# Performance work log

Hardware: AMD Instinct MI355X
Metric: run time of the kernel (lower is better)

## Reference

```python
import jax, jax.numpy as jnp
import numpy as np

N = 50000      # nodes
E = 1_000_000  # edges (avg degree 20)
D = 64         # hidden dim
L = 3          # num dynamics layers
LN_EPS = 1e-5


def layernorm(h, g, b):
    mu = jnp.mean(h, axis=-1, keepdims=True)
    var = jnp.mean(jnp.square(h - mu), axis=-1, keepdims=True)
    return (h - mu) * jax.lax.rsqrt(var + LN_EPS) * g + b


def transformer_conv(h, src, dst, Wq, bq, Wk, bk, Wv, bv, Ws, bs):
    # PyG TransformerConv, heads=1, concat=False, beta=False, root_weight=True
    n = h.shape[0]
    d = Wq.shape[1]
    q = h @ Wq + bq            # [N, D] queries (dst side)
    k = h @ Wk + bk            # [N, D] keys   (src side)
    v = h @ Wv + bv            # [N, D] values (src side)
    logits = jnp.sum(q[dst] * k[src], axis=-1) / jnp.sqrt(jnp.asarray(d, h.dtype))  # [E]
    # segment softmax over incoming edges of each dst node
    m = jax.ops.segment_max(logits, dst, num_segments=n)      # [N]
    e = jnp.exp(logits - m[dst])                               # [E]
    s = jax.ops.segment_sum(e, dst, num_segments=n)            # [N]
    a = e / s[dst]                                             # [E]
    agg = jax.ops.segment_sum(a[:, None] * v[src], dst, num_segments=n)  # [N, D]
    return agg + h @ Ws + bs   # root/skip connection


def setup_inputs() -> dict:
    key = jax.random.key(0)
    ks = jax.random.split(key, 24)
    w = lambda k, shape: (jax.random.normal(k, shape, jnp.float32) * 0.05)
    inp = {
        "x": jax.random.normal(ks[0], (N, D), jnp.float32),
        "edge_index": jax.random.randint(ks[1], (2, E), 0, N, jnp.int32),
        # input_proj conv params
        "Wq0": w(ks[2], (D, D)), "bq0": w(ks[3], (D,)),
        "Wk0": w(ks[4], (D, D)), "bk0": w(ks[5], (D,)),
        "Wv0": w(ks[6], (D, D)), "bv0": w(ks[7], (D,)),
        "Ws0": w(ks[8], (D, D)), "bs0": w(ks[9], (D,)),
        "ln0_g": jnp.ones((D,), jnp.float32), "ln0_b": jnp.zeros((D,), jnp.float32),
        # stacked dynamics conv params [L, ...]
        "Wq": w(ks[10], (L, D, D)), "bq": w(ks[11], (L, D)),
        "Wk": w(ks[12], (L, D, D)), "bk": w(ks[13], (L, D)),
        "Wv": w(ks[14], (L, D, D)), "bv": w(ks[15], (L, D)),
        "Ws": w(ks[16], (L, D, D)), "bs": w(ks[17], (L, D)),
        "ln_g": jnp.ones((L, D), jnp.float32), "ln_b": jnp.zeros((L, D), jnp.float32),
    }
    return inp


def reference(x, edge_index, Wq0, bq0, Wk0, bk0, Wv0, bv0, Ws0, bs0, ln0_g, ln0_b,
              Wq, bq, Wk, bk, Wv, bv, Ws, bs, ln_g, ln_b):
    src, dst = edge_index[0], edge_index[1]
    h = transformer_conv(x, src, dst, Wq0, bq0, Wk0, bk0, Wv0, bv0, Ws0, bs0)
    h = jax.nn.relu(layernorm(h, ln0_g, ln0_b))
    # dropout is identity in eval mode
    for i in range(L):
        hi = transformer_conv(h, src, dst, Wq[i], bq[i], Wk[i], bk[i],
                              Wv[i], bv[i], Ws[i], bs[i])
        h = jax.nn.relu(layernorm(hi + h, ln_g[i], ln_b[i]))
    return h
```

## Files before the change

### kernel.cpp

```cpp
#include <hip/hip_runtime.h>
#include <math.h>


#define DD 64
#define NB_HIST 256

typedef __attribute__((ext_vector_type(8))) _Float16 h8;
typedef __attribute__((ext_vector_type(2))) _Float16 h2;
typedef __attribute__((ext_vector_type(4))) float f32x4;

__device__ __forceinline__ unsigned short f2h(float f) {
    union { _Float16 h; unsigned short u; } c;
    c.h = (_Float16)f;
    return c.u;
}
__device__ __forceinline__ h2 u2h2(unsigned u) {
    union { unsigned u; h2 h; } c; c.u = u; return c.h;
}
__device__ __forceinline__ unsigned pk2u(float a, float b) {
    union { decltype(__builtin_amdgcn_cvt_pkrtz(0.f, 0.f)) h; unsigned u; } c;
    c.h = __builtin_amdgcn_cvt_pkrtz(a, b);
    return c.u;
}
__device__ __forceinline__ float h2dot(h2 a, h2 b, float c) {
#if __has_builtin(__builtin_amdgcn_fdot2)
    return __builtin_amdgcn_fdot2(a, b, c, false);
#else
    return fmaf((float)a[0], (float)b[0], fmaf((float)a[1], (float)b[1], c));
#endif
}

__global__ __launch_bounds__(1024) void hist_blk(const int* __restrict__ dst,
                                                 unsigned* __restrict__ cb,
                                                 int E, int nbw) {
    extern __shared__ unsigned hist[];
    int blk = blockIdx.x;
    for (int w = threadIdx.x; w < nbw; w += blockDim.x) hist[w] = 0;
    __syncthreads();
    int chunk = (E + gridDim.x - 1) / gridDim.x;
    int beg = blk * chunk;
    int end = min(E, beg + chunk);
    for (int e = beg + (int)threadIdx.x; e < end; e += blockDim.x) {
        int d = dst[e];
        atomicAdd(&hist[d >> 1], (d & 1) ? 0x10000u : 1u);
    }
    __syncthreads();
    unsigned* out = cb + (size_t)blk * nbw;
    for (int w = threadIdx.x; w < nbw; w += blockDim.x) out[w] = hist[w];
}

__global__ __launch_bounds__(256) void prefix_blk(unsigned* __restrict__ cb,
                                                  int* __restrict__ counts,
                                                  int nbw, int n) {
    int w = blockIdx.x * blockDim.x + threadIdx.x;
    if (w >= nbw) return;
    unsigned acc = 0;
#pragma unroll 1
    for (int c = 0; c < NB_HIST; c += 16) {
        unsigned t[16];
#pragma unroll
        for (int j = 0; j < 16; ++j) t[j] = cb[(size_t)(c + j) * nbw + w];
#pragma unroll
        for (int j = 0; j < 16; ++j) {
            unsigned v = t[j];
            cb[(size_t)(c + j) * nbw + w] = acc;
            acc += v;
        }
    }
    counts[2 * w] = (int)(acc & 0xffffu);
    int b1 = 2 * w + 1;
    if (b1 < n) counts[b1] = (int)(acc >> 16);
}

__global__ __launch_bounds__(1024) void scan_local(const int* __restrict__ counts,
                                                   int* __restrict__ localscan,
                                                   int* __restrict__ blockSums, int n) {
    __shared__ int sh[1024];
    int i = blockIdx.x * 1024 + threadIdx.x;
    int val = (i < n) ? counts[i] : 0;
    sh[threadIdx.x] = val;
    __syncthreads();
    for (int off = 1; off < 1024; off <<= 1) {
        int t = (threadIdx.x >= off) ? sh[threadIdx.x - off] : 0;
        __syncthreads();
        sh[threadIdx.x] += t;
        __syncthreads();
    }
    if (i < n) localscan[i] = sh[threadIdx.x] - val;
    if (threadIdx.x == 1023) blockSums[blockIdx.x] = sh[1023];
}

__global__ __launch_bounds__(64) void scan_tops(int* __restrict__ blockSums, int nb) {
    int i = threadIdx.x;
    int val = (i < nb) ? blockSums[i] : 0;
    int s = val;
#pragma unroll
    for (int off = 1; off < 64; off <<= 1) {
        int t = __shfl_up(s, off, 64);
        if (i >= off) s += t;
    }
    if (i < nb) blockSums[i] = s - val;
}

__global__ void emit_rowptr(const int* __restrict__ localscan,
                            const int* __restrict__ blockSums,
                            int* __restrict__ row_ptr, int n, int E) {
    int i = blockIdx.x * blockDim.x + threadIdx.x;
    if (i < n) row_ptr[i] = localscan[i] + blockSums[i >> 10];
    if (i == 0) row_ptr[n] = E;
}

__global__ __launch_bounds__(1024) void scatter2(const int* __restrict__ src,
                                                 const int* __restrict__ dst,
                                                 const unsigned* __restrict__ cb,
                                                 const int* __restrict__ row_ptr,
                                                 int* __restrict__ col, int E, int nbw) {
    extern __shared__ unsigned hist[];
    int blk = blockIdx.x;
    for (int w = threadIdx.x; w < nbw; w += blockDim.x) hist[w] = 0;
    __syncthreads();
    const unsigned* pref = cb + (size_t)blk * nbw;
    int chunk = (E + gridDim.x - 1) / gridDim.x;
    int beg = blk * chunk;
    int end = min(E, beg + chunk);
    for (int e = beg + (int)threadIdx.x; e < end; e += blockDim.x) {
        int d = dst[e];
        unsigned sh = (unsigned)(d & 1) * 16u;
        unsigned old = atomicAdd(&hist[d >> 1], 1u << sh);
        unsigned lr = (old >> sh) & 0xffffu;
        unsigned pre = (pref[d >> 1] >> sh) & 0xffffu;
        int slot = row_ptr[d] + (int)pre + (int)lr;
        __builtin_nontemporal_store(src[e] << 8, &col[slot]);
    }
}

__global__ void prep_all(const float* __restrict__ x, unsigned short* __restrict__ hbf,
                         int nD,
                         const float* __restrict__ W0, const float* __restrict__ W1,
                         const float* __restrict__ W2, const float* __restrict__ W3,
                         const float* __restrict__ Wqs, const float* __restrict__ Wks,
                         const float* __restrict__ Wvs, const float* __restrict__ Wss,
                         unsigned short* __restrict__ Wt) {
    int i = blockIdx.x * blockDim.x + threadIdx.x;
    if (i < nD) { hbf[i] = f2h(x[i]); return; }
    int id = i - nD;
    if (id >= 16 * 4096) return;
    int mat = id >> 12, rem = id & 4095;
    int nn = rem >> 6, kk = rem & 63;
    int layer = mat >> 2, wh = mat & 3;
    const float* W;
    if (layer == 0) W = wh == 0 ? W0 : wh == 1 ? W1 : wh == 2 ? W2 : W3;
    else {
        const float* base = wh == 0 ? Wqs : wh == 1 ? Wks : wh == 2 ? Wvs : Wss;
        W = base + (size_t)(layer - 1) * 4096;
    }
    float val = W[kk * 64 + nn];
    if (wh == 0) val *= 0.125f;
    Wt[id] = f2h(val);
}

__global__ __launch_bounds__(256) void gemm_mfma(
    const unsigned short* __restrict__ hbf, const unsigned short* __restrict__ Wt,
    const float* __restrict__ Bq, const float* __restrict__ Bk,
    const float* __restrict__ Bv, const float* __restrict__ Bs,
    const float* __restrict__ hprev,
    unsigned short* __restrict__ qO, unsigned short* __restrict__ kvO,
    unsigned short* __restrict__ sO, int ntiles) {
    int lane = threadIdx.x & 63;
    int wave = threadIdx.x >> 6;
    int ml = lane & 15, ql = lane >> 4;

    const unsigned short* W = Wt + wave * 4096;
    h8 wfrag[4][2];
#pragma unroll
    for (int t = 0; t < 4; ++t)
#pragma unroll
        for (int kh = 0; kh < 2; ++kh)
            wfrag[t][kh] = *(const h8*)(W + (t * 16 + ml) * 64 + kh * 32 + ql * 8);

    const float* bias = wave == 0 ? Bq : wave == 1 ? Bk : wave == 2 ? Bv : Bs;
    float4 bias4[4];
#pragma unroll
    for (int t = 0; t < 4; ++t) {
        bias4[t] = *(const float4*)(bias + t * 16 + ql * 4);
        if (wave == 0) {
            bias4[t].x *= 0.125f; bias4[t].y *= 0.125f;
            bias4[t].z *= 0.125f; bias4[t].w *= 0.125f;
        }
    }

    for (int tile = blockIdx.x; tile < ntiles; tile += gridDim.x) {
        int node0 = tile * 16;
        h8 hfrag[2];
#pragma unroll
        for (int kh = 0; kh < 2; ++kh)
            hfrag[kh] = *(const h8*)(hbf + (size_t)(node0 + ml) * 64 + kh * 32 + ql * 8);
        f32x4 acc[4];
#pragma unroll
        for (int t = 0; t < 4; ++t) {
            acc[t][0] = bias4[t].x; acc[t][1] = bias4[t].y;
            acc[t][2] = bias4[t].z; acc[t][3] = bias4[t].w;
        }
#pragma unroll
        for (int t = 0; t < 4; ++t)
#pragma unroll
            for (int kh = 0; kh < 2; ++kh)
                acc[t] = __builtin_amdgcn_mfma_f32_16x16x32_f16(
                    wfrag[t][kh], hfrag[kh], acc[t], 0, 0, 0);

        size_t rowe = (size_t)(node0 + ml) * 64;
        if (wave == 0) {
#pragma unroll
            for (int t = 0; t < 4; ++t) {
                uint2 st;
                st.x = pk2u(acc[t][0], acc[t][1]);
                st.y = pk2u(acc[t][2], acc[t][3]);
                *(uint2*)(qO + rowe + t * 16 + ql * 4) = st;
            }
        } else if (wave == 3) {
#pragma unroll
            for (int t = 0; t < 4; ++t) {
                float4 st = {acc[t][0], acc[t][1], acc[t][2], acc[t][3]};
                if (hprev) {
                    float4 h4 = *(const float4*)(hprev + rowe + t * 16 + ql * 4);
                    st.x += h4.x; st.y += h4.y; st.z += h4.z; st.w += h4.w;
                }
                uint2 sp;
                sp.x = pk2u(st.x, st.y);
                sp.y = pk2u(st.z, st.w);
                *(uint2*)(sO + rowe + t * 16 + ql * 4) = sp;
            }
        } else {
            size_t kve = (size_t)(node0 + ml) * 128 + (wave == 2 ? 64 : 0);
#pragma unroll
            for (int t = 0; t < 4; ++t) {
                uint2 st;
                st.x = pk2u(acc[t][0], acc[t][1]);
                st.y = pk2u(acc[t][2], acc[t][3]);
                *(uint2*)(kvO + kve + t * 16 + ql * 4) = st;
            }
        }
    }
}

#define EDGE_COMP(KU, VU) do {                                                 \
    float d = h2dot(u2h2(qu.x), u2h2((KU).x), 0.0f);                           \
    d = h2dot(u2h2(qu.y), u2h2((KU).y), d);                                    \
    d = h2dot(u2h2(qu.z), u2h2((KU).z), d);                                    \
    d = h2dot(u2h2(qu.w), u2h2((KU).w), d);                                    \
    d += __shfl_xor(d, 1); d += __shfl_xor(d, 2); d += __shfl_xor(d, 4);       \
    float p = __expf(d); ssum += p;                                            \
    h2 v0 = u2h2((VU).x), v1 = u2h2((VU).y), v2 = u2h2((VU).z), v3 = u2h2((VU).w); \
    aa.x = fmaf((float)v0[0], p, aa.x); aa.y = fmaf((float)v0[1], p, aa.y);    \
    aa.z = fmaf((float)v1[0], p, aa.z); aa.w = fmaf((float)v1[1], p, aa.w);    \
    ab.x = fmaf((float)v2[0], p, ab.x); ab.y = fmaf((float)v2[1], p, ab.y);    \
    ab.z = fmaf((float)v3[0], p, ab.z); ab.w = fmaf((float)v3[1], p, ab.w);    \
} while (0)

__global__ __launch_bounds__(256) void attn_agg_ln(
    const unsigned short* __restrict__ qh, const unsigned short* __restrict__ kv,
    const unsigned short* __restrict__ sk,
    const int* __restrict__ row_ptr, const int* __restrict__ col,
    const float* __restrict__ g, const float* __restrict__ b,
    float* __restrict__ out, unsigned short* __restrict__ hbf_out, int n) {
    int node = blockIdx.x * 4 + (threadIdx.x >> 6);
    int lane = threadIdx.x & 63;
    if (node >= n) return;
    int grp = lane >> 3;
    int qi = lane & 7;

    size_t ro = (size_t)node * DD + qi * 8;
    uint4 qu = *(const uint4*)(qh + ro);
    uint4 su = *(const uint4*)(sk + ro);
    int beg = row_ptr[node], end = row_ptr[node + 1];

    float ssum = 0.0f;
    float4 aa = {0.f, 0.f, 0.f, 0.f}, ab = {0.f, 0.f, 0.f, 0.f};
    const char* kvb = (const char*)kv;

    int e = beg + grp;
    int cv0 = (e < end) ? col[e] : -1;
    int cv1 = (e + 8 < end) ? col[e + 8] : -1;
    int cv2 = (e + 16 < end) ? col[e + 16] : -1;
    int cv3 = (e + 24 < end) ? col[e + 24] : -1;
    for (int e0 = beg; e0 < end; e0 += 32) {
        bool a0 = cv0 >= 0, a1 = cv1 >= 0, a2 = cv2 >= 0, a3 = cv3 >= 0;
        uint4 ku0, vu0, ku1, vu1, ku2, vu2, ku3, vu3;
        if (a0) { const uint4* kp = (const uint4*)(kvb + cv0) + qi; ku0 = kp[0]; vu0 = kp[8]; }
        if (a1) { const uint4* kp = (const uint4*)(kvb + cv1) + qi; ku1 = kp[0]; vu1 = kp[8]; }
        if (a2) { const uint4* kp = (const uint4*)(kvb + cv2) + qi; ku2 = kp[0]; vu2 = kp[8]; }
        if (a3) { const uint4* kp = (const uint4*)(kvb + cv3) + qi; ku3 = kp[0]; vu3 = kp[8]; }
        e += 32;
        cv0 = (e < end) ? col[e] : -1;
        cv1 = (e + 8 < end) ? col[e + 8] : -1;
        cv2 = (e + 16 < end) ? col[e + 16] : -1;
        cv3 = (e + 24 < end) ? col[e + 24] : -1;
        if (a0) EDGE_COMP(ku0, vu0);
        if (a1) EDGE_COMP(ku1, vu1);
        if (a2) EDGE_COMP(ku2, vu2);
        if (a3) EDGE_COMP(ku3, vu3);
    }

#pragma unroll
    for (int off = 8; off <= 32; off <<= 1) {
        ssum += __shfl_xor(ssum, off);
        aa.x += __shfl_xor(aa.x, off); aa.y += __shfl_xor(aa.y, off);
        aa.z += __shfl_xor(aa.z, off); aa.w += __shfl_xor(aa.w, off);
        ab.x += __shfl_xor(ab.x, off); ab.y += __shfl_xor(ab.y, off);
        ab.z += __shfl_xor(ab.z, off); ab.w += __shfl_xor(ab.w, off);
    }
    float inv = (end > beg) ? 1.0f / ssum : 0.0f;
    aa.x *= inv; aa.y *= inv; aa.z *= inv; aa.w *= inv;
    ab.x *= inv; ab.y *= inv; ab.z *= inv; ab.w *= inv;

    {
        h2 t0 = u2h2(su.x), t1 = u2h2(su.y), t2 = u2h2(su.z), t3 = u2h2(su.w);
        aa.x += (float)t0[0]; aa.y += (float)t0[1];
        aa.z += (float)t1[0]; aa.w += (float)t1[1];
        ab.x += (float)t2[0]; ab.y += (float)t2[1];
        ab.z += (float)t3[0]; ab.w += (float)t3[1];
    }

    float s1 = aa.x + aa.y + aa.z + aa.w + ab.x + ab.y + ab.z + ab.w;
    s1 += __shfl_xor(s1, 1);
    s1 += __shfl_xor(s1, 2);
    s1 += __shfl_xor(s1, 4);
    float mu = s1 * (1.0f / DD);
    float dx0 = aa.x - mu, dx1 = aa.y - mu, dx2 = aa.z - mu, dx3 = aa.w - mu;
    float dx4 = ab.x - mu, dx5 = ab.y - mu, dx6 = ab.z - mu, dx7 = ab.w - mu;
    float s2v = dx0 * dx0 + dx1 * dx1 + dx2 * dx2 + dx3 * dx3
              + dx4 * dx4 + dx5 * dx5 + dx6 * dx6 + dx7 * dx7;
    s2v += __shfl_xor(s2v, 1);
    s2v += __shfl_xor(s2v, 2);
    s2v += __shfl_xor(s2v, 4);
    float var = s2v * (1.0f / DD);
    float is = rsqrtf(var + 1e-5f);
    float4 g4a = *(const float4*)(g + qi * 8);
    float4 g4b = *(const float4*)(g + qi * 8 + 4);
    float4 b4a = *(const float4*)(b + qi * 8);
    float4 b4b = *(const float4*)(b + qi * 8 + 4);
    float4 ya, yb;
    ya.x = fmaxf(dx0 * is * g4a.x + b4a.x, 0.0f);
    ya.y = fmaxf(dx1 * is * g4a.y + b4a.y, 0.0f);
    ya.z = fmaxf(dx2 * is * g4a.z + b4a.z, 0.0f);
    ya.w = fmaxf(dx3 * is * g4a.w + b4a.w, 0.0f);
    yb.x = fmaxf(dx4 * is * g4b.x + b4b.x, 0.0f);
    yb.y = fmaxf(dx5 * is * g4b.y + b4b.y, 0.0f);
    yb.z = fmaxf(dx6 * is * g4b.z + b4b.z, 0.0f);
    yb.w = fmaxf(dx7 * is * g4b.w + b4b.w, 0.0f);
    if (grp == 0) {
        *(float4*)(out + ro) = ya;
        *(float4*)(out + ro + 4) = yb;
        uint4 hv;
        hv.x = pk2u(ya.x, ya.y);
        hv.y = pk2u(ya.z, ya.w);
        hv.z = pk2u(yb.x, yb.y);
        hv.w = pk2u(yb.z, yb.w);
        *(uint4*)(hbf_out + ro) = hv;
    }
}

extern "C" void kernel_launch(void* const* d_in, const int* in_sizes, int n_in,
                              void* d_out, int out_size, void* d_ws, size_t ws_size,
                              hipStream_t stream) {
    const int D = DD;
    const float* x = (const float*)d_in[0];
    const int n = in_sizes[0] / D;
    const int* ei = (const int*)d_in[1];
    const int E = in_sizes[1] / 2;
    const int* srcp = ei;
    const int* dstp = ei + E;
    const int nbw = (n + 1) / 2;

    static bool s_attr = false;
    if (!s_attr) {
        s_attr = true;
        (void)hipFuncSetAttribute((const void*)hist_blk,
                                  hipFuncAttributeMaxDynamicSharedMemorySize, 102400);
        (void)hipFuncSetAttribute((const void*)scatter2,
                                  hipFuncAttributeMaxDynamicSharedMemorySize, 102400);
    }

    char* wsp = (char*)d_ws;
    auto take = [&](size_t bytes) {
        char* p = wsp;
        wsp += (bytes + 255) & ~(size_t)255;
        return (void*)p;
    };
    int* counts    = (int*)take((size_t)n * 4);
    int* row_ptr   = (int*)take((size_t)(n + 1) * 4);
    unsigned* cb   = (unsigned*)take((size_t)NB_HIST * nbw * 4);
    int* col       = (int*)take((size_t)E * 4);
    int* localscan = (int*)take((size_t)n * 4);
    int* blockSums = (int*)take((size_t)1024 * 4);
    size_t fsz = (size_t)n * D * 4;
    unsigned short* qb  = (unsigned short*)take(fsz / 2);
    unsigned short* kvb = (unsigned short*)take(fsz);
    unsigned short* sb  = (unsigned short*)take(fsz / 2);
    float* hA           = (float*)take(fsz);
    float* hB           = (float*)take(fsz);
    unsigned short* hbf = (unsigned short*)take(fsz / 2);
    unsigned short* Wt  = (unsigned short*)take((size_t)16 * 4096 * 2);

    int tb = 256;
    size_t ldsH = (size_t)nbw * 4;
    int nbScan = (n + 1023) / 1024;
    hist_blk<<<NB_HIST, 1024, ldsH, stream>>>(dstp, cb, E, nbw);
    prefix_blk<<<(nbw + tb - 1) / tb, tb, 0, stream>>>(cb, counts, nbw, n);
    scan_local<<<nbScan, 1024, 0, stream>>>(counts, localscan, blockSums, n);
    scan_tops<<<1, 64, 0, stream>>>(blockSums, nbScan);
    emit_rowptr<<<(n + tb - 1) / tb, tb, 0, stream>>>(localscan, blockSums, row_ptr, n, E);
    scatter2<<<NB_HIST, 1024, ldsH, stream>>>(srcp, dstp, cb, row_ptr, col, E, nbw);

    int prep_total = n * D + 16 * 4096;
    prep_all<<<(prep_total + 255) / 256, 256, 0, stream>>>(
        x, hbf, n * D,
        (const float*)d_in[2], (const float*)d_in[4], (const float*)d_in[6],
        (const float*)d_in[8], (const float*)d_in[12], (const float*)d_in[14],
        (const float*)d_in[16], (const float*)d_in[18], Wt);

    int ntiles = n / 16;
    int nba = (n + 3) / 4;
    const float* h = x;
    for (int layer = 0; layer < 4; ++layer) {
        const float *bq_, *bk_, *bv_, *bs_, *g_, *b_;
        if (layer == 0) {
            bq_ = (const float*)d_in[3];  bk_ = (const float*)d_in[5];
            bv_ = (const float*)d_in[7];  bs_ = (const float*)d_in[9];
            g_  = (const float*)d_in[10]; b_  = (const float*)d_in[11];
        } else {
            int i = layer - 1;
            bq_ = (const float*)d_in[13] + (size_t)i * D;
            bk_ = (const float*)d_in[15] + (size_t)i * D;
            bv_ = (const float*)d_in[17] + (size_t)i * D;
            bs_ = (const float*)d_in[19] + (size_t)i * D;
            g_  = (const float*)d_in[20] + (size_t)i * D;
            b_  = (const float*)d_in[21] + (size_t)i * D;
        }
        gemm_mfma<<<512, 256, 0, stream>>>(hbf, Wt + (size_t)layer * 4 * 4096,
                                           bq_, bk_, bv_, bs_,
                                           layer == 0 ? nullptr : h,
                                           qb, kvb, sb, ntiles);
        float* hout = (layer == 3) ? (float*)d_out : ((layer & 1) ? hB : hA);
        attn_agg_ln<<<nba, 256, 0, stream>>>(qb, kvb, sb, row_ptr, col,
                                             g_, b_, hout, hbf, n);
        h = hout;
    }
}
```

Measured before the change: 377.1 us.

## Read residual from fp16 hidden buffer, drop fp32 intermediates, halve edge unroll

The skip/residual add in the GEMM now reads the fp16 hidden copy instead of the fp32 previous output. That lets the attention kernel skip its fp32 writes for all but the last layer, and the fp32 ping-pong buffers are removed. The edge loop unroll drops from 4 to 2 in flight per group, and the GEMM grid doubles to 1024 blocks. This cuts memory traffic and register pressure, at the cost of a residual with lower precision and less memory-level parallelism in the gather.

```diff
diff --git a/kernel.cpp b/kernel.cpp
--- a/kernel.cpp
+++ b/kernel.cpp
@@ -163,7 +163,7 @@
     const unsigned short* __restrict__ hbf, const unsigned short* __restrict__ Wt,
     const float* __restrict__ Bq, const float* __restrict__ Bk,
     const float* __restrict__ Bv, const float* __restrict__ Bs,
-    const float* __restrict__ hprev,
+    int with_res,
     unsigned short* __restrict__ qO, unsigned short* __restrict__ kvO,
     unsigned short* __restrict__ sO, int ntiles) {
     int lane = threadIdx.x & 63;
@@ -221,9 +221,11 @@
 #pragma unroll
             for (int t = 0; t < 4; ++t) {
                 float4 st = {acc[t][0], acc[t][1], acc[t][2], acc[t][3]};
-                if (hprev) {
-                    float4 h4 = *(const float4*)(hprev + rowe + t * 16 + ql * 4);
-                    st.x += h4.x; st.y += h4.y; st.z += h4.z; st.w += h4.w;
+                if (with_res) {
+                    uint2 hv = *(const uint2*)(hbf + rowe + t * 16 + ql * 4);
+                    h2 r0 = u2h2(hv.x), r1 = u2h2(hv.y);
+                    st.x += (float)r0[0]; st.y += (float)r0[1];
+                    st.z += (float)r1[0]; st.w += (float)r1[1];
                 }
                 uint2 sp;
                 sp.x = pk2u(st.x, st.y);
@@ -281,24 +283,16 @@
     int e = beg + grp;
     int cv0 = (e < end) ? col[e] : -1;
     int cv1 = (e + 8 < end) ? col[e + 8] : -1;
-    int cv2 = (e + 16 < end) ? col[e + 16] : -1;
-    int cv3 = (e + 24 < end) ? col[e + 24] : -1;
-    for (int e0 = beg; e0 < end; e0 += 32) {
-        bool a0 = cv0 >= 0, a1 = cv1 >= 0, a2 = cv2 >= 0, a3 = cv3 >= 0;
-        uint4 ku0, vu0, ku1, vu1, ku2, vu2, ku3, vu3;
+    for (int e0 = beg; e0 < end; e0 += 16) {
+        bool a0 = cv0 >= 0, a1 = cv1 >= 0;
+        uint4 ku0, vu0, ku1, vu1;
         if (a0) { const uint4* kp = (const uint4*)(kvb + cv0) + qi; ku0 = kp[0]; vu0 = kp[8]; }
         if (a1) { const uint4* kp = (const uint4*)(kvb + cv1) + qi; ku1 = kp[0]; vu1 = kp[8]; }
-        if (a2) { const uint4* kp = (const uint4*)(kvb + cv2) + qi; ku2 = kp[0]; vu2 = kp[8]; }
-        if (a3) { const uint4* kp = (const uint4*)(kvb + cv3) + qi; ku3 = kp[0]; vu3 = kp[8]; }
-        e += 32;
+        e += 16;
         cv0 = (e < end) ? col[e] : -1;
         cv1 = (e + 8 < end) ? col[e + 8] : -1;
-        cv2 = (e + 16 < end) ? col[e + 16] : -1;
-        cv3 = (e + 24 < end) ? col[e + 24] : -1;
         if (a0) EDGE_COMP(ku0, vu0);
         if (a1) EDGE_COMP(ku1, vu1);
-        if (a2) EDGE_COMP(ku2, vu2);
-        if (a3) EDGE_COMP(ku3, vu3);
     }
 
 #pragma unroll
@@ -349,8 +343,10 @@
     yb.z = fmaxf(dx6 * is * g4b.z + b4b.z, 0.0f);
     yb.w = fmaxf(dx7 * is * g4b.w + b4b.w, 0.0f);
     if (grp == 0) {
-        *(float4*)(out + ro) = ya;
-        *(float4*)(out + ro + 4) = yb;
+        if (out) {
+            *(float4*)(out + ro) = ya;
+            *(float4*)(out + ro + 4) = yb;
+        }
         uint4 hv;
         hv.x = pk2u(ya.x, ya.y);
         hv.y = pk2u(ya.z, ya.w);
@@ -397,8 +393,6 @@
     unsigned short* qb  = (unsigned short*)take(fsz / 2);
     unsigned short* kvb = (unsigned short*)take(fsz);
     unsigned short* sb  = (unsigned short*)take(fsz / 2);
-    float* hA           = (float*)take(fsz);
-    float* hB           = (float*)take(fsz);
     unsigned short* hbf = (unsigned short*)take(fsz / 2);
     unsigned short* Wt  = (unsigned short*)take((size_t)16 * 4096 * 2);
 
@@ -421,7 +415,6 @@
 
     int ntiles = n / 16;
     int nba = (n + 3) / 4;
-    const float* h = x;
     for (int layer = 0; layer < 4; ++layer) {
         const float *bq_, *bk_, *bv_, *bs_, *g_, *b_;
         if (layer == 0) {
@@ -437,13 +430,12 @@
             g_  = (const float*)d_in[20] + (size_t)i * D;
             b_  = (const float*)d_in[21] + (size_t)i * D;
         }
-        gemm_mfma<<<512, 256, 0, stream>>>(hbf, Wt + (size_t)layer * 4 * 4096,
-                                           bq_, bk_, bv_, bs_,
-                                           layer == 0 ? nullptr : h,
-                                           qb, kvb, sb, ntiles);
-        float* hout = (layer == 3) ? (float*)d_out : ((layer & 1) ? hB : hA);
-        attn_agg_ln<<<nba, 256, 0, stream>>>(qb, kvb, sb, row_ptr, col,
-                                             g_, b_, hout, hbf, n);
-        h = hout;
-    }
-}
+        gemm_mfma<<<1024, 256, 0, stream>>>(hbf, Wt + (size_t)layer * 4 * 4096,
+                                            bq_, bk_, bv_, bs_,
+                                            layer == 0 ? 0 : 1,
+                                            qb, kvb, sb, ntiles);
+        attn_agg_ln<<<nba, 256, 0, stream>>>(qb, kvb, sb, row_ptr, col, g_, b_,
+                                             layer == 3 ? (float*)d_out : nullptr,
+                                             hbf, n);
+    }
+}
```

Measured after the change: 375.4 us. No clear change (-0.5%).
